# Kernel optimization log

Hardware: AMD Instinct MI355X
Metric: run time of the kernel (lower is better)

## Reference

```python
import jax, jax.numpy as jnp
import numpy as np

N = 50000
E = 800000
TEXT_VOCAB = 7000
ACTION_DIM = 64
MAX_POS = 5120
POS_DIM = 128   # edge encoder out_dim
NODE_DIM = 128  # text_out 64 + type_out 64
EDGE_DIM = 128
H1 = 256
OUT = 32
NEG_SLOPE = 0.2


def _pos_table():
    # sinusoidal table, [MAX_POS+1, POS_DIM]; even cols = cos, odd cols = sin
    positions = np.arange(0, MAX_POS + 1, dtype=np.float32)
    inv_freq = 1.0 / (10000.0 ** (np.arange(0.0, POS_DIM, 2.0, dtype=np.float32) / POS_DIM))
    si = np.outer(positions, inv_freq)
    tab = np.zeros((MAX_POS + 1, POS_DIM), dtype=np.float32)
    tab[:, 1::2] = np.sin(si)
    tab[:, 0::2] = np.cos(si)
    return jnp.asarray(tab)


def setup_inputs() -> dict:
    key = jax.random.key(0)
    ks = jax.random.split(key, 32)
    ri = jax.random.randint
    nrm = lambda k, s, scale=0.05: (jax.random.normal(k, s, dtype=jnp.float32) * scale)
    x = jnp.stack([ri(ks[0], (N,), 0, TEXT_VOCAB + 1, dtype=jnp.int32),
                   ri(ks[1], (N,), 0, 3, dtype=jnp.int32)], axis=-1)
    edge_index = ri(ks[2], (2, E), 0, N, dtype=jnp.int32)
    edge_attr = jnp.stack([ri(ks[3], (E,), 0, 3, dtype=jnp.int32),
                           ri(ks[4], (E,), 0, MAX_POS + 1, dtype=jnp.int32)], axis=-1)
    d = {
        "x": x, "edge_index": edge_index, "edge_attr": edge_attr,
        "text_emb": nrm(ks[5], (TEXT_VOCAB + 1, 64), 1.0),
        "type_emb": nrm(ks[6], (3, 64), 1.0),
        "flow_emb": nrm(ks[7], (3, EDGE_DIM), 1.0),
        "pos_table": _pos_table(),
        "pos_W": nrm(ks[8], (POS_DIM, POS_DIM)), "pos_b": nrm(ks[9], (POS_DIM,)),
        "c1_Wl": nrm(ks[10], (NODE_DIM, H1)), "c1_bl": nrm(ks[11], (H1,)),
        "c1_Wr": nrm(ks[12], (NODE_DIM, H1)), "c1_br": nrm(ks[13], (H1,)),
        "c1_We": nrm(ks[14], (EDGE_DIM, H1)), "c1_att": nrm(ks[15], (H1,)),
        "c1_bias": nrm(ks[16], (H1,)),
        "c2_Wl": nrm(ks[17], (H1, OUT)), "c2_bl": nrm(ks[18], (OUT,)),
        "c2_Wr": nrm(ks[19], (H1, OUT)), "c2_br": nrm(ks[20], (OUT,)),
        "c2_We": nrm(ks[21], (EDGE_DIM, OUT)), "c2_att": nrm(ks[22], (OUT,)),
        "c2_bias": nrm(ks[23], (OUT,)),
        "policy_W": nrm(ks[24], (OUT, ACTION_DIM), 0.2), "policy_b": nrm(ks[25], (ACTION_DIM,)),
    }
    return d


def gatv2(h, src, dst, ea, Wl, bl, Wr, br, We, att, bias, n):
    # PyG GATv2Conv, heads=1, add_self_loops=True, fill_value='mean'
    loop_attr = jnp.broadcast_to(ea.mean(0), (n, ea.shape[1]))
    s = jnp.concatenate([src, jnp.arange(n, dtype=src.dtype)])
    d = jnp.concatenate([dst, jnp.arange(n, dtype=dst.dtype)])
    ea_full = jnp.concatenate([ea, loop_attr], axis=0)
    xl = h @ Wl + bl  # messages (source side)
    xr = h @ Wr + br  # destination side
    m = xl[s] + xr[d] + ea_full @ We          # [E+n, F]
    e = jnp.where(m > 0, m, NEG_SLOPE * m) @ att  # per-edge logit [E+n]
    emax = jax.ops.segment_max(e, d, num_segments=n)
    a = jnp.exp(e - emax[d])
    denom = jax.ops.segment_sum(a, d, num_segments=n)
    alpha = a / denom[d]
    return jax.ops.segment_sum(alpha[:, None] * xl[s], d, num_segments=n) + bias


def reference(x, edge_index, edge_attr, text_emb, type_emb, flow_emb, pos_table,
              pos_W, pos_b,
              c1_Wl, c1_bl, c1_Wr, c1_br, c1_We, c1_att, c1_bias,
              c2_Wl, c2_bl, c2_Wr, c2_br, c2_We, c2_att, c2_bias,
              policy_W, policy_b):
    # NodeEncoder: concat of text and type embeddings -> [N, 128]
    h = jnp.concatenate([text_emb[x[:, 0]], type_emb[x[:, 1]]], axis=-1)
    # EdgeEncoder: flow embedding + linear(position sinusoid embedding)
    pos = edge_attr[:, 1]
    pos = jnp.where(pos > MAX_POS, pos, MAX_POS)  # faithful to original .where usage
    pos = jnp.clip(pos, 0, MAX_POS)
    ea = flow_emb[edge_attr[:, 0]] + (pos_table[pos] @ pos_W + pos_b)  # [E, 128]
    src, dst = edge_index[0], edge_index[1]
    h = gatv2(h, src, dst, ea, c1_Wl, c1_bl, c1_Wr, c1_br, c1_We, c1_att, c1_bias, h.shape[0])
    h = gatv2(h, src, dst, ea, c2_Wl, c2_bl, c2_Wr, c2_br, c2_We, c2_att, c2_bias, h.shape[0])
    g = h.mean(0)  # [32] graph readout
    logits = g @ policy_W + policy_b
    return jax.nn.softmax(logits, axis=-1)
```

## Files before the change

### kernel.cpp

```cpp
#include <hip/hip_runtime.h>

#define NEG_SLOPE 0.2f

typedef __attribute__((ext_vector_type(8))) short bf16x8;
typedef __attribute__((ext_vector_type(4))) float f32x4;

static __device__ __forceinline__ float lrelu(float m) {
    return fmaf(0.4f, fabsf(m), 0.6f * m);
}

static __device__ __forceinline__ float wsum64(float v) {
#pragma unroll
    for (int off = 32; off >= 1; off >>= 1) v += __shfl_xor(v, off, 64);
    return v;
}
static __device__ __forceinline__ float wsum32(float v) {
#pragma unroll
    for (int off = 16; off >= 1; off >>= 1) v += __shfl_xor(v, off, 64);
    return v;
}
static __device__ __forceinline__ float wmax64(float v) {
#pragma unroll
    for (int off = 32; off >= 1; off >>= 1) v = fmaxf(v, __shfl_xor(v, off, 64));
    return v;
}

static __device__ __forceinline__ unsigned short bf16r(float a) {
    unsigned int u = __float_as_uint(a);
    return (unsigned short)((u + 0x7FFFu + ((u >> 16) & 1u)) >> 16);
}
static __device__ __forceinline__ unsigned int bf16pack(float a, float b) {
    unsigned int ua = __float_as_uint(a);
    ua = (ua + 0x7FFFu + ((ua >> 16) & 1u)) >> 16;
    unsigned int ub = __float_as_uint(b);
    ub = (ub + 0x7FFFu + ((ub >> 16) & 1u)) & 0xFFFF0000u;
    return ua | ub;
}
static __device__ __forceinline__ float bfld(unsigned short s) {
    return __uint_as_float((unsigned int)s << 16);
}
static __device__ __forceinline__ float4 bf16x4_to_f4(uint2 u) {
    float4 v;
    v.x = __uint_as_float(u.x << 16);
    v.y = __uint_as_float(u.x & 0xFFFF0000u);
    v.z = __uint_as_float(u.y << 16);
    v.w = __uint_as_float(u.y & 0xFFFF0000u);
    return v;
}

static __device__ __forceinline__ float ldot4(const float4 xs, const float4 pre,
                                              const float4 av) {
    float q;
    q  = lrelu(xs.x + pre.x) * av.x;
    q += lrelu(xs.y + pre.y) * av.y;
    q += lrelu(xs.z + pre.z) * av.z;
    q += lrelu(xs.w + pre.w) * av.w;
    return q;
}

__global__ void k_zero_all(int* __restrict__ cntw, int n, int* __restrict__ cnt3,
                           int* __restrict__ gsum) {
    int i = blockIdx.x * blockDim.x + threadIdx.x;
    if (i < n) cntw[i] = 0;
    if (i < 4) cnt3[i] = 0;
    if (i < 32) gsum[i] = 0;
}

__global__ void k_edges(const int* __restrict__ ei, const int* __restrict__ ea,
                        int* __restrict__ cnt, int* __restrict__ cnt3, int E) {
    __shared__ int sh3[3];
    if (threadIdx.x < 3) sh3[threadIdx.x] = 0;
    __syncthreads();
    int e = blockIdx.x * blockDim.x + threadIdx.x;
    if (e < E) {
        atomicAdd(&cnt[ei[E + e]], 1);
        int f = ea[2 * e];
        f = f < 0 ? 0 : (f > 2 ? 2 : f);
        atomicAdd(&sh3[f], 1);
    }
    __syncthreads();
    if (threadIdx.x < 3) atomicAdd(&cnt3[threadIdx.x], sh3[threadIdx.x]);
}

__global__ void k_prep(const float* __restrict__ pos_table, const float* __restrict__ pos_W,
                       const float* __restrict__ pos_b, const float* __restrict__ flow_emb,
                       const float* __restrict__ We1, const float* __restrict__ We2,
                       const int* __restrict__ cnt3,
                       float* __restrict__ eaW1, float* __restrict__ loopW1,
                       float* __restrict__ eaW2, float* __restrict__ loopW2, int E) {
    __shared__ float posc[128];
    __shared__ float lv[128];
    int t = threadIdx.x;
    if (t < 128) {
        const float* row = pos_table + 5120 * 128;
        float a = pos_b[t];
        for (int k = 0; k < 128; ++k) a += row[k] * pos_W[k * 128 + t];
        posc[t] = a;
        float invE = 1.0f / (float)E;
        lv[t] = ((float)cnt3[0] * flow_emb[t] + (float)cnt3[1] * flow_emb[128 + t] +
                 (float)cnt3[2] * flow_emb[256 + t]) * invE + a;
    }
    __syncthreads();
    {
        int j = t;
        float a0 = 0.f, a1 = 0.f, a2 = 0.f, al = 0.f;
        for (int k = 0; k < 128; ++k) {
            float w = We1[k * 256 + j];
            float pc = posc[k];
            a0 += (flow_emb[k] + pc) * w;
            a1 += (flow_emb[128 + k] + pc) * w;
            a2 += (flow_emb[256 + k] + pc) * w;
            al += lv[k] * w;
        }
        eaW1[j] = a0; eaW1[256 + j] = a1; eaW1[512 + j] = a2; loopW1[j] = al;
    }
    if (t < 32) {
        int j = t;
        float a0 = 0.f, a1 = 0.f, a2 = 0.f, al = 0.f;
        for (int k = 0; k < 128; ++k) {
            float w = We2[k * 32 + j];
            float pc = posc[k];
            a0 += (flow_emb[k] + pc) * w;
            a1 += (flow_emb[128 + k] + pc) * w;
            a2 += (flow_emb[256 + k] + pc) * w;
            al += lv[k] * w;
        }
        eaW2[j] = a0; eaW2[32 + j] = a1; eaW2[64 + j] = a2; loopW2[j] = al;
    }
}

__global__ void k_prepW(const float* __restrict__ Wl1, const float* __restrict__ Wr1,
                        const float* __restrict__ Wl2, const float* __restrict__ Wr2,
                        unsigned short* __restrict__ Bt1, unsigned short* __restrict__ Bt2) {
    int i = blockIdx.x * blockDim.x + threadIdx.x;
    if (i < 512 * 128) {
        int nn = i >> 7, k = i & 127;
        float v = (nn < 256) ? Wl1[(size_t)k * 256 + nn] : Wr1[(size_t)k * 256 + nn - 256];
        Bt1[i] = bf16r(v);
    } else {
        int j = i - 512 * 128;
        if (j < 64 * 256) {
            int nn = j >> 8, k = j & 255;
            float v = (nn < 32) ? Wl2[(size_t)k * 32 + nn] : Wr2[(size_t)k * 32 + nn - 32];
            Bt2[j] = bf16r(v);
        }
    }
}

__global__ __launch_bounds__(256) void k_scan_block(const int* __restrict__ cnt,
                                                    int* __restrict__ rowptr,
                                                    int* __restrict__ bsum, int n) {
    __shared__ int sh[256];
    int b = blockIdx.x, t = threadIdx.x;
    int base = b * 1024 + t * 4;
    int v0 = base + 0 < n ? cnt[base + 0] : 0;
    int v1 = base + 1 < n ? cnt[base + 1] : 0;
    int v2 = base + 2 < n ? cnt[base + 2] : 0;
    int v3 = base + 3 < n ? cnt[base + 3] : 0;
    int tot = v0 + v1 + v2 + v3;
    sh[t] = tot;
    __syncthreads();
    for (int off = 1; off < 256; off <<= 1) {
        int x = (t >= off) ? sh[t - off] : 0;
        __syncthreads();
        sh[t] += x;
        __syncthreads();
    }
    int excl = (t > 0) ? sh[t - 1] : 0;
    if (base + 0 < n) rowptr[base + 0] = excl;
    if (base + 1 < n) rowptr[base + 1] = excl + v0;
    if (base + 2 < n) rowptr[base + 2] = excl + v0 + v1;
    if (base + 3 < n) rowptr[base + 3] = excl + v0 + v1 + v2;
    if (t == 255) bsum[b] = sh[255];
}

__global__ void k_scan_top(int* __restrict__ bsum, int* __restrict__ rowptr, int nb, int n) {
    if (threadIdx.x == 0 && blockIdx.x == 0) {
        int run = 0;
        for (int b = 0; b < nb; ++b) { int x = bsum[b]; bsum[b] = run; run += x; }
        rowptr[n] = run;
    }
}

__global__ void k_scan_add(int* __restrict__ rowptr, const int* __restrict__ bsum,
                           int* __restrict__ wptr, int n) {
    int i = blockIdx.x * blockDim.x + threadIdx.x;
    if (i < n) {
        int v = rowptr[i] + bsum[i >> 10];
        rowptr[i] = v;
        wptr[i] = v;
    }
}

__global__ void k_scatter(const int* __restrict__ ei, const int* __restrict__ ea,
                          int* __restrict__ wptr, int* __restrict__ packed, int E) {
    int e = blockIdx.x * blockDim.x + threadIdx.x;
    if (e >= E) return;
    int s = ei[e], d = ei[E + e];
    int f = ea[2 * e];
    f = f < 0 ? 0 : (f > 2 ? 2 : f);
    int p = atomicAdd(&wptr[d], 1);
    packed[p] = (s & 0xFFFF) | (f << 16);
}

__global__ __launch_bounds__(256) void k_gemm1(const int* __restrict__ x,
        const float* __restrict__ text_emb, const float* __restrict__ type_emb,
        const unsigned short* __restrict__ Bt,
        const float* __restrict__ bl, const float* __restrict__ br,
        unsigned short* __restrict__ xc, int n) {
    __shared__ unsigned short Ash[64][136];
    __shared__ unsigned short Bsh[128][136];
    int t = threadIdx.x;
    int node0 = blockIdx.x * 64;
    for (int i = t; i < 64 * 128; i += 256) {
        int r = i >> 7, cc = i & 127;
        int nd = node0 + r;
        float v = 0.f;
        if (nd < n)
            v = (cc < 64) ? text_emb[(size_t)x[nd * 2] * 64 + cc]
                          : type_emb[(size_t)x[nd * 2 + 1] * 64 + (cc - 64)];
        Ash[r][cc] = bf16r(v);
    }
    int wave = t >> 6, lane = t & 63;
    int m = lane & 15, q = lane >> 4;
    for (int nb = 0; nb < 4; ++nb) {
        __syncthreads();
        for (int i = t; i < 128 * 16; i += 256) {
            int r = i >> 4, cs = i & 15;
            uint4 v = ((const uint4*)(Bt + (size_t)(nb * 128 + r) * 128))[cs];
            *(uint4*)&Bsh[r][cs * 8] = v;
        }
        __syncthreads();
        f32x4 acc[8];
#pragma unroll
        for (int nt = 0; nt < 8; ++nt) acc[nt] = (f32x4){0.f, 0.f, 0.f, 0.f};
#pragma unroll
        for (int k = 0; k < 128; k += 32) {
            bf16x8 a = *(const bf16x8*)&Ash[wave * 16 + m][k + q * 8];
#pragma unroll
            for (int nt = 0; nt < 8; ++nt) {
                bf16x8 b = *(const bf16x8*)&Bsh[nt * 16 + m][k + q * 8];
                acc[nt] = __builtin_amdgcn_mfma_f32_16x16x32_bf16(a, b, acc[nt], 0, 0, 0);
            }
        }
#pragma unroll
        for (int r = 0; r < 4; ++r) {
            int node = node0 + wave * 16 + q * 4 + r;
            if (node < n) {
                unsigned short* rowp = xc + (size_t)node * 512 + nb * 128 + m;
#pragma unroll
                for (int nt = 0; nt < 8; ++nt) {
                    int ng = nb * 128 + nt * 16 + m;
                    float bv = (ng < 256) ? bl[ng] : br[ng - 256];
                    rowp[nt * 16] = bf16r(acc[nt][r] + bv);
                }
            }
        }
    }
}

__global__ __launch_bounds__(256) void k_gemm2(const unsigned short* __restrict__ h2b,
        const unsigned short* __restrict__ Bt,
        const float* __restrict__ bl, const float* __restrict__ br,
        unsigned short* __restrict__ xc, int n) {
    __shared__ unsigned short Ash[32][264];
    __shared__ unsigned short Bsh[64][264];
    int t = threadIdx.x;
    int node0 = blockIdx.x * 32;
    for (int i = t; i < 32 * 32; i += 256) {
        int r = i >> 5, cs = i & 31;
        int nd = node0 + r;
        uint4 v = make_uint4(0u, 0u, 0u, 0u);
        if (nd < n) v = ((const uint4*)(h2b + (size_t)nd * 256))[cs];
        *(uint4*)&Ash[r][cs * 8] = v;
    }
    for (int i = t; i < 64 * 32; i += 256) {
        int r = i >> 5, cs = i & 31;
        uint4 v = ((const uint4*)(Bt + (size_t)r * 256))[cs];
        *(uint4*)&Bsh[r][cs * 8] = v;
    }
    __syncthreads();
    int wave = t >> 6, lane = t & 63;
    int m = lane & 15, q = lane >> 4;
    int mrow = (wave >> 1) * 16;
    int nh   = (wave & 1) * 32;
    f32x4 acc[2];
    acc[0] = (f32x4){0.f, 0.f, 0.f, 0.f};
    acc[1] = (f32x4){0.f, 0.f, 0.f, 0.f};
#pragma unroll
    for (int k = 0; k < 256; k += 32) {
        bf16x8 a = *(const bf16x8*)&Ash[mrow + m][k + q * 8];
#pragma unroll
        for (int nt = 0; nt < 2; ++nt) {
            bf16x8 b = *(const bf16x8*)&Bsh[nh + nt * 16 + m][k + q * 8];
            acc[nt] = __builtin_amdgcn_mfma_f32_16x16x32_bf16(a, b, acc[nt], 0, 0, 0);
        }
    }
#pragma unroll
    for (int r = 0; r < 4; ++r) {
        int node = node0 + mrow + q * 4 + r;
        if (node < n) {
#pragma unroll
            for (int nt = 0; nt < 2; ++nt) {
                int ng = nh + nt * 16 + m;
                float bv = (ng < 32) ? bl[ng] : br[ng - 32];
                xc[(size_t)node * 64 + ng] = bf16r(acc[nt][r] + bv);
            }
        }
    }
}

__global__ __launch_bounds__(256) void k_gat256(const unsigned short* __restrict__ xc1,
        const int* __restrict__ rowptr, const int* __restrict__ packed,
        const float* __restrict__ eaW, const float* __restrict__ loopW,
        const float* __restrict__ att, const float* __restrict__ bias,
        unsigned short* __restrict__ h2b, int n) {
    int wid = (blockIdx.x * blockDim.x + threadIdx.x) >> 6;
    int lane = threadIdx.x & 63;
    if (wid >= n) return;
    int d = wid;
    int c = lane * 4;
    float4 xld = bf16x4_to_f4(((const uint2*)(xc1 + (size_t)d * 512))[lane]);
    float4 xrd = bf16x4_to_f4(((const uint2*)(xc1 + (size_t)d * 512 + 256))[lane]);
    float4 av  = *(const float4*)(att + c);
    float4 r0 = *(const float4*)(eaW + c);
    float4 r1 = *(const float4*)(eaW + 256 + c);
    float4 r2 = *(const float4*)(eaW + 512 + c);
    r0.x += xrd.x; r0.y += xrd.y; r0.z += xrd.z; r0.w += xrd.w;
    r1.x += xrd.x; r1.y += xrd.y; r1.z += xrd.z; r1.w += xrd.w;
    r2.x += xrd.x; r2.y += xrd.y; r2.z += xrd.z; r2.w += xrd.w;
    float4 lw = *(const float4*)(loopW + c);
    float4 sl; sl.x = xrd.x + lw.x; sl.y = xrd.y + lw.y;
    sl.z = xrd.z + lw.z; sl.w = xrd.w + lw.w;
    float q = wsum64(ldot4(xld, sl, av));
    float wself = __expf(q);
    float den = wself;
    float4 acc;
    acc.x = wself * xld.x; acc.y = wself * xld.y;
    acc.z = wself * xld.z; acc.w = wself * xld.w;

    int p0 = rowptr[d], p1 = rowptr[d + 1];
    int p = p0;
    for (; p + 4 <= p1; p += 4) {
        int pk0 = packed[p], pk1 = packed[p + 1];
        int pk2 = packed[p + 2], pk3 = packed[p + 3];
        uint2 u0 = ((const uint2*)(xc1 + (size_t)(pk0 & 0xFFFF) * 512))[lane];
        uint2 u1 = ((const uint2*)(xc1 + (size_t)(pk1 & 0xFFFF) * 512))[lane];
        uint2 u2 = ((const uint2*)(xc1 + (size_t)(pk2 & 0xFFFF) * 512))[lane];
        uint2 u3 = ((const uint2*)(xc1 + (size_t)(pk3 & 0xFFFF) * 512))[lane];
        float4 xs0 = bf16x4_to_f4(u0);
        float4 xs1 = bf16x4_to_f4(u1);
        float4 xs2 = bf16x4_to_f4(u2);
        float4 xs3 = bf16x4_to_f4(u3);
        int f0 = pk0 >> 16, f1 = pk1 >> 16, f2 = pk2 >> 16, f3 = pk3 >> 16;
        float4 pr0 = (f0 == 0) ? r0 : ((f0 == 1) ? r1 : r2);
        float4 pr1 = (f1 == 0) ? r0 : ((f1 == 1) ? r1 : r2);
        float4 pr2 = (f2 == 0) ? r0 : ((f2 == 1) ? r1 : r2);
        float4 pr3 = (f3 == 0) ? r0 : ((f3 == 1) ? r1 : r2);
        float q0 = ldot4(xs0, pr0, av);
        float q1 = ldot4(xs1, pr1, av);
        float q2 = ldot4(xs2, pr2, av);
        float q3 = ldot4(xs3, pr3, av);
#pragma unroll
        for (int off = 32; off >= 1; off >>= 1) {
            q0 += __shfl_xor(q0, off, 64);
            q1 += __shfl_xor(q1, off, 64);
            q2 += __shfl_xor(q2, off, 64);
            q3 += __shfl_xor(q3, off, 64);
        }
        float w0 = __expf(q0), w1 = __expf(q1);
        float w2 = __expf(q2), w3 = __expf(q3);
        den += (w0 + w1) + (w2 + w3);
        acc.x += w0 * xs0.x + w1 * xs1.x + w2 * xs2.x + w3 * xs3.x;
        acc.y += w0 * xs0.y + w1 * xs1.y + w2 * xs2.y + w3 * xs3.y;
        acc.z += w0 * xs0.z + w1 * xs1.z + w2 * xs2.z + w3 * xs3.z;
        acc.w += w0 * xs0.w + w1 * xs1.w + w2 * xs2.w + w3 * xs3.w;
    }
    for (; p < p1; ++p) {
        int pk = packed[p];
        float4 xs = bf16x4_to_f4(((const uint2*)(xc1 + (size_t)(pk & 0xFFFF) * 512))[lane]);
        int f = pk >> 16;
        float4 pr = (f == 0) ? r0 : ((f == 1) ? r1 : r2);
        float qq = wsum64(ldot4(xs, pr, av));
        float w = __expf(qq);
        den += w;
        acc.x += w * xs.x; acc.y += w * xs.y; acc.z += w * xs.z; acc.w += w * xs.w;
    }
    float inv = 1.f / den;
    float4 bv = *(const float4*)(bias + c);
    float4 o;
    o.x = acc.x * inv + bv.x; o.y = acc.y * inv + bv.y;
    o.z = acc.z * inv + bv.z; o.w = acc.w * inv + bv.w;
    ((uint2*)(h2b + (size_t)d * 256))[lane] =
        make_uint2(bf16pack(o.x, o.y), bf16pack(o.z, o.w));
}

__global__ __launch_bounds__(256) void k_gat32(const unsigned short* __restrict__ xc2,
        const int* __restrict__ rowptr, const int* __restrict__ packed,
        const float* __restrict__ eaW, const float* __restrict__ loopW,
        const float* __restrict__ att, const float* __restrict__ bias,
        float* __restrict__ out, int n) {
    int wid = (blockIdx.x * blockDim.x + threadIdx.x) >> 6;
    int lane = threadIdx.x & 63;
    if (wid >= n) return;
    int d = wid;
    int half = lane >> 5;
    int c = lane & 31;
    float xld = bfld(xc2[(size_t)d * 64 + c]);
    float xrd = bfld(xc2[(size_t)d * 64 + 32 + c]);
    float av = att[c];
    float r0 = eaW[c] + xrd, r1 = eaW[32 + c] + xrd, r2 = eaW[64 + c] + xrd;
    float den = 0.f, acc = 0.f;
    if (half == 0) {
        float lw = loopW[c];
        float q = wsum32(lrelu(xld + xrd + lw) * av);
        float wself = __expf(q);
        den = wself;
        acc = wself * xld;
    }
    int p0 = rowptr[d], p1 = rowptr[d + 1];
    int p = p0 + half;
    for (; p + 2 < p1; p += 4) {
        int pkA = packed[p], pkB = packed[p + 2];
        float xsA = bfld(xc2[(size_t)(pkA & 0xFFFF) * 64 + c]);
        float xsB = bfld(xc2[(size_t)(pkB & 0xFFFF) * 64 + c]);
        int fA = pkA >> 16, fB = pkB >> 16;
        float prA = (fA == 0) ? r0 : ((fA == 1) ? r1 : r2);
        float prB = (fB == 0) ? r0 : ((fB == 1) ? r1 : r2);
        float qA = lrelu(xsA + prA) * av;
        float qB = lrelu(xsB + prB) * av;
#pragma unroll
        for (int off = 16; off >= 1; off >>= 1) {
            qA += __shfl_xor(qA, off, 64);
            qB += __shfl_xor(qB, off, 64);
        }
        float wA = __expf(qA), wB = __expf(qB);
        den += wA + wB;
        acc += wA * xsA + wB * xsB;
    }
    for (; p < p1; p += 2) {
        int pk = packed[p];
        float xs = bfld(xc2[(size_t)(pk & 0xFFFF) * 64 + c]);
        int f = pk >> 16;
        float pr = (f == 0) ? r0 : ((f == 1) ? r1 : r2);
        float q = wsum32(lrelu(xs + pr) * av);
        float w = __expf(q);
        den += w;
        acc += w * xs;
    }
    den += __shfl_xor(den, 32, 64);
    acc += __shfl_xor(acc, 32, 64);
    if (lane < 32) out[(size_t)d * 32 + c] = acc / den + bias[c];
}

__global__ __launch_bounds__(256) void k_mean(const float* __restrict__ out2,
                                              float* __restrict__ gsum, int n) {
    __shared__ float sh[256];
    int t = threadIdx.x;
    int c = t & 31, g = t >> 5;
    float acc = 0.f;
    for (int nd = blockIdx.x * 8 + g; nd < n; nd += gridDim.x * 8)
        acc += out2[(size_t)nd * 32 + c];
    sh[t] = acc;
    __syncthreads();
    if (t < 32) {
        float s2 = 0.f;
#pragma unroll
        for (int gg = 0; gg < 8; ++gg) s2 += sh[gg * 32 + c];
        atomicAdd(&gsum[c], s2);
    }
}

__global__ void k_final(const float* __restrict__ gsum, const float* __restrict__ policy_W,
                        const float* __restrict__ policy_b, float* __restrict__ out, int n) {
    int t = threadIdx.x;
    float invN = 1.0f / (float)n;
    float acc = policy_b[t];
    for (int cc = 0; cc < 32; ++cc) acc += gsum[cc] * invN * policy_W[cc * 64 + t];
    float mx = wmax64(acc);
    float ex = __expf(acc - mx);
    float s = wsum64(ex);
    out[t] = ex / s;
}

extern "C" void kernel_launch(void* const* d_in, const int* in_sizes, int n_in,
                              void* d_out, int out_size, void* d_ws, size_t ws_size,
                              hipStream_t stream) {
    const int* x          = (const int*)d_in[0];
    const int* edge_index = (const int*)d_in[1];
    const int* edge_attr  = (const int*)d_in[2];
    const float* text_emb = (const float*)d_in[3];
    const float* type_emb = (const float*)d_in[4];
    const float* flow_emb = (const float*)d_in[5];
    const float* pos_table= (const float*)d_in[6];
    const float* pos_W    = (const float*)d_in[7];
    const float* pos_b    = (const float*)d_in[8];
    const float* c1_Wl    = (const float*)d_in[9];
    const float* c1_bl    = (const float*)d_in[10];
    const float* c1_Wr    = (const float*)d_in[11];
    const float* c1_br    = (const float*)d_in[12];
    const float* c1_We    = (const float*)d_in[13];
    const float* c1_att   = (const float*)d_in[14];
    const float* c1_bias  = (const float*)d_in[15];
    const float* c2_Wl    = (const float*)d_in[16];
    const float* c2_bl    = (const float*)d_in[17];
    const float* c2_Wr    = (const float*)d_in[18];
    const float* c2_br    = (const float*)d_in[19];
    const float* c2_We    = (const float*)d_in[20];
    const float* c2_att   = (const float*)d_in[21];
    const float* c2_bias  = (const float*)d_in[22];
    const float* policy_W = (const float*)d_in[23];
    const float* policy_b = (const float*)d_in[24];
    float* out = (float*)d_out;

    const int N = in_sizes[0] / 2;
    const int E = in_sizes[1] / 2;

    char* base = (char*)d_ws;
    size_t off = 0;
    auto alloc = [&](size_t bytes) -> void* {
        void* p = base + off;
        off = (off + bytes + 255) & ~(size_t)255;
        return p;
    };
    unsigned short* xc1  = (unsigned short*)alloc((size_t)N * 512 * 2);
    unsigned short* h2b  = (unsigned short*)alloc((size_t)N * 256 * 2);
    unsigned short* xc2  = (unsigned short*)alloc((size_t)N * 64 * 2);
    float*          out2 = (float*)alloc((size_t)N * 32 * 4);
    unsigned short* Bt1  = (unsigned short*)alloc((size_t)512 * 128 * 2);
    unsigned short* Bt2  = (unsigned short*)alloc((size_t)64 * 256 * 2);
    int*            cntw   = (int*)alloc((size_t)N * 4);
    int*            rowptr = (int*)alloc((size_t)(N + 1) * 4);
    int*            packed = (int*)alloc((size_t)E * 4);
    int*            bsum   = (int*)alloc(64 * 4);
    int*            cnt3   = (int*)alloc(4 * 4);
    float*          eaW1   = (float*)alloc(768 * 4);
    float*          loopW1 = (float*)alloc(256 * 4);
    float*          eaW2   = (float*)alloc(96 * 4);
    float*          loopW2 = (float*)alloc(32 * 4);
    float*          gsum   = (float*)alloc(32 * 4);

    k_zero_all<<<(N + 255) / 256, 256, 0, stream>>>(cntw, N, cnt3, (int*)gsum);

    k_edges<<<(E + 255) / 256, 256, 0, stream>>>(edge_index, edge_attr, cntw, cnt3, E);
    k_prep<<<1, 256, 0, stream>>>(pos_table, pos_W, pos_b, flow_emb, c1_We, c2_We,
                                  cnt3, eaW1, loopW1, eaW2, loopW2, E);
    k_prepW<<<(512 * 128 + 64 * 256 + 255) / 256, 256, 0, stream>>>(
        c1_Wl, c1_Wr, c2_Wl, c2_Wr, Bt1, Bt2);

    int nb = (N + 1023) / 1024;
    k_scan_block<<<nb, 256, 0, stream>>>(cntw, rowptr, bsum, N);
    k_scan_top<<<1, 64, 0, stream>>>(bsum, rowptr, nb, N);
    k_scan_add<<<(N + 255) / 256, 256, 0, stream>>>(rowptr, bsum, cntw, N);
    k_scatter<<<(E + 255) / 256, 256, 0, stream>>>(edge_index, edge_attr, cntw, packed, E);

    k_gemm1<<<(N + 63) / 64, 256, 0, stream>>>(x, text_emb, type_emb, Bt1,
                                               c1_bl, c1_br, xc1, N);
    k_gat256<<<(N + 3) / 4, 256, 0, stream>>>(xc1, rowptr, packed, eaW1, loopW1,
                                              c1_att, c1_bias, h2b, N);

    k_gemm2<<<(N + 31) / 32, 256, 0, stream>>>(h2b, Bt2, c2_bl, c2_br, xc2, N);
    k_gat32<<<(N + 3) / 4, 256, 0, stream>>>(xc2, rowptr, packed, eaW2, loopW2,
                                             c2_att, c2_bias, out2, N);

    k_mean<<<256, 256, 0, stream>>>(out2, gsum, N);
    k_final<<<1, 64, 0, stream>>>(gsum, policy_W, policy_b, out, N);
}
```

Before: 447.0 us.

## Bucket CSR by destination and flow type; restructure GAT edge loops

Builds the CSR keyed on (destination, flow type) so each GAT kernel walks three sub-ranges with a fixed edge-attribute term per range. This removes the per-edge flow select and packed-index decoding, so only the raw source index is stored. It also folds the leaky-ReLU constants into scaled attention vectors, and reorganises the 32-wide GAT to process four edges per wavefront with 16 lanes each. Weight prep is merged into one launch and zeroing becomes a single memset. The trade-off is a scan three times longer and extra loop overhead for short per-type segments.

```diff
diff --git a/kernel.cpp b/kernel.cpp
--- a/kernel.cpp
+++ b/kernel.cpp
@@ -5,18 +5,9 @@
 typedef __attribute__((ext_vector_type(8))) short bf16x8;
 typedef __attribute__((ext_vector_type(4))) float f32x4;
 
-static __device__ __forceinline__ float lrelu(float m) {
-    return fmaf(0.4f, fabsf(m), 0.6f * m);
-}
-
 static __device__ __forceinline__ float wsum64(float v) {
 #pragma unroll
     for (int off = 32; off >= 1; off >>= 1) v += __shfl_xor(v, off, 64);
-    return v;
-}
-static __device__ __forceinline__ float wsum32(float v) {
-#pragma unroll
-    for (int off = 16; off >= 1; off >>= 1) v += __shfl_xor(v, off, 64);
     return v;
 }
 static __device__ __forceinline__ float wmax64(float v) {
@@ -35,9 +26,6 @@
     unsigned int ub = __float_as_uint(b);
     ub = (ub + 0x7FFFu + ((ub >> 16) & 1u)) & 0xFFFF0000u;
     return ua | ub;
-}
-static __device__ __forceinline__ float bfld(unsigned short s) {
-    return __uint_as_float((unsigned int)s << 16);
 }
 static __device__ __forceinline__ float4 bf16x4_to_f4(uint2 u) {
     float4 v;
@@ -48,46 +36,60 @@
     return v;
 }
 
-static __device__ __forceinline__ float ldot4(const float4 xs, const float4 pre,
-                                              const float4 av) {
-    float q;
-    q  = lrelu(xs.x + pre.x) * av.x;
-    q += lrelu(xs.y + pre.y) * av.y;
-    q += lrelu(xs.z + pre.z) * av.z;
-    q += lrelu(xs.w + pre.w) * av.w;
+static __device__ __forceinline__ float sdot4(const float4 xs, const float4 pre,
+                                              const float4 av6, const float4 av4) {
+    float m0 = xs.x + pre.x, m1 = xs.y + pre.y;
+    float m2 = xs.z + pre.z, m3 = xs.w + pre.w;
+    float q = av6.x * m0 + av4.x * fabsf(m0);
+    q = fmaf(av6.y, m1, q); q = fmaf(av4.y, fabsf(m1), q);
+    q = fmaf(av6.z, m2, q); q = fmaf(av4.z, fabsf(m2), q);
+    q = fmaf(av6.w, m3, q); q = fmaf(av4.w, fabsf(m3), q);
     return q;
 }
 
-__global__ void k_zero_all(int* __restrict__ cntw, int n, int* __restrict__ cnt3,
-                           int* __restrict__ gsum) {
-    int i = blockIdx.x * blockDim.x + threadIdx.x;
-    if (i < n) cntw[i] = 0;
-    if (i < 4) cnt3[i] = 0;
-    if (i < 32) gsum[i] = 0;
-}
-
 __global__ void k_edges(const int* __restrict__ ei, const int* __restrict__ ea,
-                        int* __restrict__ cnt, int* __restrict__ cnt3, int E) {
+                        int* __restrict__ cntF, int* __restrict__ cnt3, int E) {
     __shared__ int sh3[3];
     if (threadIdx.x < 3) sh3[threadIdx.x] = 0;
     __syncthreads();
     int e = blockIdx.x * blockDim.x + threadIdx.x;
     if (e < E) {
-        atomicAdd(&cnt[ei[E + e]], 1);
+        int dd = ei[E + e];
         int f = ea[2 * e];
         f = f < 0 ? 0 : (f > 2 ? 2 : f);
+        atomicAdd(&cntF[dd * 3 + f], 1);
         atomicAdd(&sh3[f], 1);
     }
     __syncthreads();
     if (threadIdx.x < 3) atomicAdd(&cnt3[threadIdx.x], sh3[threadIdx.x]);
 }
 
-__global__ void k_prep(const float* __restrict__ pos_table, const float* __restrict__ pos_W,
-                       const float* __restrict__ pos_b, const float* __restrict__ flow_emb,
-                       const float* __restrict__ We1, const float* __restrict__ We2,
-                       const int* __restrict__ cnt3,
-                       float* __restrict__ eaW1, float* __restrict__ loopW1,
-                       float* __restrict__ eaW2, float* __restrict__ loopW2, int E) {
+__global__ void k_prep_all(const float* __restrict__ pos_table, const float* __restrict__ pos_W,
+                           const float* __restrict__ pos_b, const float* __restrict__ flow_emb,
+                           const float* __restrict__ We1, const float* __restrict__ We2,
+                           const int* __restrict__ cnt3,
+                           float* __restrict__ eaW1, float* __restrict__ loopW1,
+                           float* __restrict__ eaW2, float* __restrict__ loopW2,
+                           const float* __restrict__ Wl1, const float* __restrict__ Wr1,
+                           const float* __restrict__ Wl2, const float* __restrict__ Wr2,
+                           unsigned short* __restrict__ Bt1, unsigned short* __restrict__ Bt2,
+                           int E) {
+    if (blockIdx.x != 0) {
+        int i = (blockIdx.x - 1) * 256 + threadIdx.x;
+        if (i < 512 * 128) {
+            int nn = i >> 7, k = i & 127;
+            float v = (nn < 256) ? Wl1[(size_t)k * 256 + nn] : Wr1[(size_t)k * 256 + nn - 256];
+            Bt1[i] = bf16r(v);
+        } else {
+            int j = i - 512 * 128;
+            if (j < 64 * 256) {
+                int nn = j >> 8, k = j & 255;
+                float v = (nn < 32) ? Wl2[(size_t)k * 32 + nn] : Wr2[(size_t)k * 32 + nn - 32];
+                Bt2[j] = bf16r(v);
+            }
+        }
+        return;
+    }
     __shared__ float posc[128];
     __shared__ float lv[128];
     int t = threadIdx.x;
@@ -126,24 +128,6 @@
             al += lv[k] * w;
         }
         eaW2[j] = a0; eaW2[32 + j] = a1; eaW2[64 + j] = a2; loopW2[j] = al;
-    }
-}
-
-__global__ void k_prepW(const float* __restrict__ Wl1, const float* __restrict__ Wr1,
-                        const float* __restrict__ Wl2, const float* __restrict__ Wr2,
-                        unsigned short* __restrict__ Bt1, unsigned short* __restrict__ Bt2) {
-    int i = blockIdx.x * blockDim.x + threadIdx.x;
-    if (i < 512 * 128) {
-        int nn = i >> 7, k = i & 127;
-        float v = (nn < 256) ? Wl1[(size_t)k * 256 + nn] : Wr1[(size_t)k * 256 + nn - 256];
-        Bt1[i] = bf16r(v);
-    } else {
-        int j = i - 512 * 128;
-        if (j < 64 * 256) {
-            int nn = j >> 8, k = j & 255;
-            float v = (nn < 32) ? Wl2[(size_t)k * 32 + nn] : Wr2[(size_t)k * 32 + nn - 32];
-            Bt2[j] = bf16r(v);
-        }
     }
 }
 
@@ -196,11 +180,11 @@
                           int* __restrict__ wptr, int* __restrict__ packed, int E) {
     int e = blockIdx.x * blockDim.x + threadIdx.x;
     if (e >= E) return;
-    int s = ei[e], d = ei[E + e];
+    int s = ei[e], dd = ei[E + e];
     int f = ea[2 * e];
     f = f < 0 ? 0 : (f > 2 ? 2 : f);
-    int p = atomicAdd(&wptr[d], 1);
-    packed[p] = (s & 0xFFFF) | (f << 16);
+    int p = atomicAdd(&wptr[dd * 3 + f], 1);
+    packed[p] = s;
 }
 
 __global__ __launch_bounds__(256) void k_gemm1(const int* __restrict__ x,
@@ -311,7 +295,7 @@
 }
 
 __global__ __launch_bounds__(256) void k_gat256(const unsigned short* __restrict__ xc1,
-        const int* __restrict__ rowptr, const int* __restrict__ packed,
+        const int* __restrict__ rowptrF, const int* __restrict__ packed,
         const float* __restrict__ eaW, const float* __restrict__ loopW,
         const float* __restrict__ att, const float* __restrict__ bias,
         unsigned short* __restrict__ h2b, int n) {
@@ -322,135 +306,156 @@
     int c = lane * 4;
     float4 xld = bf16x4_to_f4(((const uint2*)(xc1 + (size_t)d * 512))[lane]);
     float4 xrd = bf16x4_to_f4(((const uint2*)(xc1 + (size_t)d * 512 + 256))[lane]);
-    float4 av  = *(const float4*)(att + c);
-    float4 r0 = *(const float4*)(eaW + c);
-    float4 r1 = *(const float4*)(eaW + 256 + c);
-    float4 r2 = *(const float4*)(eaW + 512 + c);
-    r0.x += xrd.x; r0.y += xrd.y; r0.z += xrd.z; r0.w += xrd.w;
-    r1.x += xrd.x; r1.y += xrd.y; r1.z += xrd.z; r1.w += xrd.w;
-    r2.x += xrd.x; r2.y += xrd.y; r2.z += xrd.z; r2.w += xrd.w;
-    float4 lw = *(const float4*)(loopW + c);
-    float4 sl; sl.x = xrd.x + lw.x; sl.y = xrd.y + lw.y;
-    sl.z = xrd.z + lw.z; sl.w = xrd.w + lw.w;
-    float q = wsum64(ldot4(xld, sl, av));
-    float wself = __expf(q);
-    float den = wself;
+    float4 av = *(const float4*)(att + c);
+    float4 av6, av4;
+    av6.x = 0.6f * av.x; av6.y = 0.6f * av.y; av6.z = 0.6f * av.z; av6.w = 0.6f * av.w;
+    av4.x = 0.4f * av.x; av4.y = 0.4f * av.y; av4.z = 0.4f * av.z; av4.w = 0.4f * av.w;
+    float den, wself;
     float4 acc;
-    acc.x = wself * xld.x; acc.y = wself * xld.y;
-    acc.z = wself * xld.z; acc.w = wself * xld.w;
-
-    int p0 = rowptr[d], p1 = rowptr[d + 1];
-    int p = p0;
-    for (; p + 4 <= p1; p += 4) {
-        int pk0 = packed[p], pk1 = packed[p + 1];
-        int pk2 = packed[p + 2], pk3 = packed[p + 3];
-        uint2 u0 = ((const uint2*)(xc1 + (size_t)(pk0 & 0xFFFF) * 512))[lane];
-        uint2 u1 = ((const uint2*)(xc1 + (size_t)(pk1 & 0xFFFF) * 512))[lane];
-        uint2 u2 = ((const uint2*)(xc1 + (size_t)(pk2 & 0xFFFF) * 512))[lane];
-        uint2 u3 = ((const uint2*)(xc1 + (size_t)(pk3 & 0xFFFF) * 512))[lane];
-        float4 xs0 = bf16x4_to_f4(u0);
-        float4 xs1 = bf16x4_to_f4(u1);
-        float4 xs2 = bf16x4_to_f4(u2);
-        float4 xs3 = bf16x4_to_f4(u3);
-        int f0 = pk0 >> 16, f1 = pk1 >> 16, f2 = pk2 >> 16, f3 = pk3 >> 16;
-        float4 pr0 = (f0 == 0) ? r0 : ((f0 == 1) ? r1 : r2);
-        float4 pr1 = (f1 == 0) ? r0 : ((f1 == 1) ? r1 : r2);
-        float4 pr2 = (f2 == 0) ? r0 : ((f2 == 1) ? r1 : r2);
-        float4 pr3 = (f3 == 0) ? r0 : ((f3 == 1) ? r1 : r2);
-        float q0 = ldot4(xs0, pr0, av);
-        float q1 = ldot4(xs1, pr1, av);
-        float q2 = ldot4(xs2, pr2, av);
-        float q3 = ldot4(xs3, pr3, av);
-#pragma unroll
-        for (int off = 32; off >= 1; off >>= 1) {
-            q0 += __shfl_xor(q0, off, 64);
-            q1 += __shfl_xor(q1, off, 64);
-            q2 += __shfl_xor(q2, off, 64);
-            q3 += __shfl_xor(q3, off, 64);
-        }
-        float w0 = __expf(q0), w1 = __expf(q1);
-        float w2 = __expf(q2), w3 = __expf(q3);
-        den += (w0 + w1) + (w2 + w3);
-        acc.x += w0 * xs0.x + w1 * xs1.x + w2 * xs2.x + w3 * xs3.x;
-        acc.y += w0 * xs0.y + w1 * xs1.y + w2 * xs2.y + w3 * xs3.y;
-        acc.z += w0 * xs0.z + w1 * xs1.z + w2 * xs2.z + w3 * xs3.z;
-        acc.w += w0 * xs0.w + w1 * xs1.w + w2 * xs2.w + w3 * xs3.w;
-    }
-    for (; p < p1; ++p) {
-        int pk = packed[p];
-        float4 xs = bf16x4_to_f4(((const uint2*)(xc1 + (size_t)(pk & 0xFFFF) * 512))[lane]);
-        int f = pk >> 16;
-        float4 pr = (f == 0) ? r0 : ((f == 1) ? r1 : r2);
-        float qq = wsum64(ldot4(xs, pr, av));
-        float w = __expf(qq);
-        den += w;
-        acc.x += w * xs.x; acc.y += w * xs.y; acc.z += w * xs.z; acc.w += w * xs.w;
+    {
+        float4 lw = *(const float4*)(loopW + c);
+        lw.x += xrd.x; lw.y += xrd.y; lw.z += xrd.z; lw.w += xrd.w;
+        float q = wsum64(sdot4(xld, lw, av6, av4));
+        wself = __expf(q);
+        den = wself;
+        acc.x = wself * xld.x; acc.y = wself * xld.y;
+        acc.z = wself * xld.z; acc.w = wself * xld.w;
+    }
+#pragma unroll 1
+    for (int f = 0; f < 3; ++f) {
+        float4 pre = *(const float4*)(eaW + f * 256 + c);
+        pre.x += xrd.x; pre.y += xrd.y; pre.z += xrd.z; pre.w += xrd.w;
+        int p = rowptrF[d * 3 + f], p1 = rowptrF[d * 3 + f + 1];
+        for (; p + 4 <= p1; p += 4) {
+            int s0 = packed[p],     s1 = packed[p + 1];
+            int s2 = packed[p + 2], s3 = packed[p + 3];
+            uint2 u0 = ((const uint2*)(xc1 + (size_t)s0 * 512))[lane];
+            uint2 u1 = ((const uint2*)(xc1 + (size_t)s1 * 512))[lane];
+            uint2 u2 = ((const uint2*)(xc1 + (size_t)s2 * 512))[lane];
+            uint2 u3 = ((const uint2*)(xc1 + (size_t)s3 * 512))[lane];
+            float4 xs0 = bf16x4_to_f4(u0);
+            float4 xs1 = bf16x4_to_f4(u1);
+            float4 xs2 = bf16x4_to_f4(u2);
+            float4 xs3 = bf16x4_to_f4(u3);
+            float q0 = sdot4(xs0, pre, av6, av4);
+            float q1 = sdot4(xs1, pre, av6, av4);
+            float q2 = sdot4(xs2, pre, av6, av4);
+            float q3 = sdot4(xs3, pre, av6, av4);
+#pragma unroll
+            for (int off = 32; off >= 1; off >>= 1) {
+                q0 += __shfl_xor(q0, off, 64);
+                q1 += __shfl_xor(q1, off, 64);
+                q2 += __shfl_xor(q2, off, 64);
+                q3 += __shfl_xor(q3, off, 64);
+            }
+            float w0 = __expf(q0), w1 = __expf(q1);
+            float w2 = __expf(q2), w3 = __expf(q3);
+            den += (w0 + w1) + (w2 + w3);
+            acc.x += w0 * xs0.x + w1 * xs1.x + w2 * xs2.x + w3 * xs3.x;
+            acc.y += w0 * xs0.y + w1 * xs1.y + w2 * xs2.y + w3 * xs3.y;
+            acc.z += w0 * xs0.z + w1 * xs1.z + w2 * xs2.z + w3 * xs3.z;
+            acc.w += w0 * xs0.w + w1 * xs1.w + w2 * xs2.w + w3 * xs3.w;
+        }
+        for (; p < p1; ++p) {
+            int s = packed[p];
+            float4 xs = bf16x4_to_f4(((const uint2*)(xc1 + (size_t)s * 512))[lane]);
+            float qq = wsum64(sdot4(xs, pre, av6, av4));
+            float w = __expf(qq);
+            den += w;
+            acc.x += w * xs.x; acc.y += w * xs.y; acc.z += w * xs.z; acc.w += w * xs.w;
+        }
     }
     float inv = 1.f / den;
     float4 bv = *(const float4*)(bias + c);
-    float4 o;
-    o.x = acc.x * inv + bv.x; o.y = acc.y * inv + bv.y;
-    o.z = acc.z * inv + bv.z; o.w = acc.w * inv + bv.w;
-    ((uint2*)(h2b + (size_t)d * 256))[lane] =
-        make_uint2(bf16pack(o.x, o.y), bf16pack(o.z, o.w));
+    float ox = fmaf(acc.x, inv, bv.x), oy = fmaf(acc.y, inv, bv.y);
+    float oz = fmaf(acc.z, inv, bv.z), ow = fmaf(acc.w, inv, bv.w);
+    ((uint2*)(h2b + (size_t)d * 256))[lane] = make_uint2(bf16pack(ox, oy), bf16pack(oz, ow));
 }
 
 __global__ __launch_bounds__(256) void k_gat32(const unsigned short* __restrict__ xc2,
-        const int* __restrict__ rowptr, const int* __restrict__ packed,
+        const int* __restrict__ rowptrF, const int* __restrict__ packed,
         const float* __restrict__ eaW, const float* __restrict__ loopW,
         const float* __restrict__ att, const float* __restrict__ bias,
         float* __restrict__ out, int n) {
     int wid = (blockIdx.x * blockDim.x + threadIdx.x) >> 6;
+    if (wid >= n) return;
     int lane = threadIdx.x & 63;
-    if (wid >= n) return;
+    int g = lane >> 4, li = lane & 15;
     int d = wid;
-    int half = lane >> 5;
-    int c = lane & 31;
-    float xld = bfld(xc2[(size_t)d * 64 + c]);
-    float xrd = bfld(xc2[(size_t)d * 64 + 32 + c]);
-    float av = att[c];
-    float r0 = eaW[c] + xrd, r1 = eaW[32 + c] + xrd, r2 = eaW[64 + c] + xrd;
-    float den = 0.f, acc = 0.f;
-    if (half == 0) {
-        float lw = loopW[c];
-        float q = wsum32(lrelu(xld + xrd + lw) * av);
+    unsigned int uxl = ((const unsigned int*)(xc2 + (size_t)d * 64))[li];
+    unsigned int uxr = ((const unsigned int*)(xc2 + (size_t)d * 64 + 32))[li];
+    float xl0 = __uint_as_float(uxl << 16), xl1 = __uint_as_float(uxl & 0xFFFF0000u);
+    float xr0 = __uint_as_float(uxr << 16), xr1 = __uint_as_float(uxr & 0xFFFF0000u);
+    float2 avv = ((const float2*)att)[li];
+    float a60 = 0.6f * avv.x, a61 = 0.6f * avv.y;
+    float a40 = 0.4f * avv.x, a41 = 0.4f * avv.y;
+    float den, acc0, acc1;
+    {
+        float2 lwv = ((const float2*)loopW)[li];
+        float m0 = xl0 + xr0 + lwv.x, m1 = xl1 + xr1 + lwv.y;
+        float q = a60 * m0 + a40 * fabsf(m0);
+        q = fmaf(a61, m1, q); q = fmaf(a41, fabsf(m1), q);
+        q += __shfl_xor(q, 1, 64); q += __shfl_xor(q, 2, 64);
+        q += __shfl_xor(q, 4, 64); q += __shfl_xor(q, 8, 64);
         float wself = __expf(q);
-        den = wself;
-        acc = wself * xld;
-    }
-    int p0 = rowptr[d], p1 = rowptr[d + 1];
-    int p = p0 + half;
-    for (; p + 2 < p1; p += 4) {
-        int pkA = packed[p], pkB = packed[p + 2];
-        float xsA = bfld(xc2[(size_t)(pkA & 0xFFFF) * 64 + c]);
-        float xsB = bfld(xc2[(size_t)(pkB & 0xFFFF) * 64 + c]);
-        int fA = pkA >> 16, fB = pkB >> 16;
-        float prA = (fA == 0) ? r0 : ((fA == 1) ? r1 : r2);
-        float prB = (fB == 0) ? r0 : ((fB == 1) ? r1 : r2);
-        float qA = lrelu(xsA + prA) * av;
-        float qB = lrelu(xsB + prB) * av;
-#pragma unroll
-        for (int off = 16; off >= 1; off >>= 1) {
-            qA += __shfl_xor(qA, off, 64);
-            qB += __shfl_xor(qB, off, 64);
-        }
-        float wA = __expf(qA), wB = __expf(qB);
-        den += wA + wB;
-        acc += wA * xsA + wB * xsB;
-    }
-    for (; p < p1; p += 2) {
-        int pk = packed[p];
-        float xs = bfld(xc2[(size_t)(pk & 0xFFFF) * 64 + c]);
-        int f = pk >> 16;
-        float pr = (f == 0) ? r0 : ((f == 1) ? r1 : r2);
-        float q = wsum32(lrelu(xs + pr) * av);
-        float w = __expf(q);
-        den += w;
-        acc += w * xs;
-    }
-    den += __shfl_xor(den, 32, 64);
-    acc += __shfl_xor(acc, 32, 64);
-    if (lane < 32) out[(size_t)d * 32 + c] = acc / den + bias[c];
+        den  = (g == 0) ? wself : 0.f;
+        acc0 = (g == 0) ? wself * xl0 : 0.f;
+        acc1 = (g == 0) ? wself * xl1 : 0.f;
+    }
+#pragma unroll 1
+    for (int f = 0; f < 3; ++f) {
+        float2 ev = ((const float2*)(eaW + f * 32))[li];
+        float pre0 = ev.x + xr0, pre1 = ev.y + xr1;
+        int pA = rowptrF[d * 3 + f], pB = rowptrF[d * 3 + f + 1];
+        int p = pA + g;
+        for (; p + 4 < pB; p += 8) {
+            int s0 = packed[p], s1 = packed[p + 4];
+            unsigned int ua = ((const unsigned int*)(xc2 + (size_t)s0 * 64))[li];
+            unsigned int ub = ((const unsigned int*)(xc2 + (size_t)s1 * 64))[li];
+            float xa0 = __uint_as_float(ua << 16), xa1 = __uint_as_float(ua & 0xFFFF0000u);
+            float xb0 = __uint_as_float(ub << 16), xb1 = __uint_as_float(ub & 0xFFFF0000u);
+            float ma0 = xa0 + pre0, ma1 = xa1 + pre1;
+            float mb0 = xb0 + pre0, mb1 = xb1 + pre1;
+            float qa = a60 * ma0 + a40 * fabsf(ma0);
+            qa = fmaf(a61, ma1, qa); qa = fmaf(a41, fabsf(ma1), qa);
+            float qb = a60 * mb0 + a40 * fabsf(mb0);
+            qb = fmaf(a61, mb1, qb); qb = fmaf(a41, fabsf(mb1), qb);
+#pragma unroll
+            for (int off = 1; off <= 8; off <<= 1) {
+                qa += __shfl_xor(qa, off, 64);
+                qb += __shfl_xor(qb, off, 64);
+            }
+            float wa = __expf(qa), wb = __expf(qb);
+            den += wa + wb;
+            acc0 = fmaf(wb, xb0, fmaf(wa, xa0, acc0));
+            acc1 = fmaf(wb, xb1, fmaf(wa, xa1, acc1));
+        }
+        for (; p < pB; p += 4) {
+            int s = packed[p];
+            unsigned int u = ((const unsigned int*)(xc2 + (size_t)s * 64))[li];
+            float x0 = __uint_as_float(u << 16), x1 = __uint_as_float(u & 0xFFFF0000u);
+            float m0 = x0 + pre0, m1 = x1 + pre1;
+            float q = a60 * m0 + a40 * fabsf(m0);
+            q = fmaf(a61, m1, q); q = fmaf(a41, fabsf(m1), q);
+            q += __shfl_xor(q, 1, 64); q += __shfl_xor(q, 2, 64);
+            q += __shfl_xor(q, 4, 64); q += __shfl_xor(q, 8, 64);
+            float w = __expf(q);
+            den += w;
+            acc0 = fmaf(w, x0, acc0);
+            acc1 = fmaf(w, x1, acc1);
+        }
+    }
+    acc0 += __shfl_xor(acc0, 16, 64); acc0 += __shfl_xor(acc0, 32, 64);
+    acc1 += __shfl_xor(acc1, 16, 64); acc1 += __shfl_xor(acc1, 32, 64);
+    den  += __shfl_xor(den, 16, 64);  den  += __shfl_xor(den, 32, 64);
+    if (g == 0) {
+        float2 bvv = ((const float2*)bias)[li];
+        float inv = 1.f / den;
+        float2 o;
+        o.x = fmaf(acc0, inv, bvv.x);
+        o.y = fmaf(acc1, inv, bvv.y);
+        ((float2*)(out + (size_t)d * 32))[li] = o;
+    }
 }
 
 __global__ __launch_bounds__(256) void k_mean(const float* __restrict__ out2,
@@ -515,6 +520,7 @@
 
     const int N = in_sizes[0] / 2;
     const int E = in_sizes[1] / 2;
+    const int n3 = 3 * N;
 
     char* base = (char*)d_ws;
     size_t off = 0;
@@ -529,38 +535,38 @@
     float*          out2 = (float*)alloc((size_t)N * 32 * 4);
     unsigned short* Bt1  = (unsigned short*)alloc((size_t)512 * 128 * 2);
     unsigned short* Bt2  = (unsigned short*)alloc((size_t)64 * 256 * 2);
-    int*            cntw   = (int*)alloc((size_t)N * 4);
-    int*            rowptr = (int*)alloc((size_t)(N + 1) * 4);
+    int*            zreg   = (int*)alloc((size_t)(n3 + 36) * 4);
+    int*            cntF   = zreg;
+    int*            cnt3   = zreg + n3;
+    float*          gsum   = (float*)(zreg + n3 + 4);
+    int*            rowptrF= (int*)alloc((size_t)(n3 + 1) * 4);
     int*            packed = (int*)alloc((size_t)E * 4);
-    int*            bsum   = (int*)alloc(64 * 4);
-    int*            cnt3   = (int*)alloc(4 * 4);
+    int*            bsum   = (int*)alloc(256 * 4);
     float*          eaW1   = (float*)alloc(768 * 4);
     float*          loopW1 = (float*)alloc(256 * 4);
     float*          eaW2   = (float*)alloc(96 * 4);
     float*          loopW2 = (float*)alloc(32 * 4);
-    float*          gsum   = (float*)alloc(32 * 4);
-
-    k_zero_all<<<(N + 255) / 256, 256, 0, stream>>>(cntw, N, cnt3, (int*)gsum);
-
-    k_edges<<<(E + 255) / 256, 256, 0, stream>>>(edge_index, edge_attr, cntw, cnt3, E);
-    k_prep<<<1, 256, 0, stream>>>(pos_table, pos_W, pos_b, flow_emb, c1_We, c2_We,
-                                  cnt3, eaW1, loopW1, eaW2, loopW2, E);
-    k_prepW<<<(512 * 128 + 64 * 256 + 255) / 256, 256, 0, stream>>>(
-        c1_Wl, c1_Wr, c2_Wl, c2_Wr, Bt1, Bt2);
-
-    int nb = (N + 1023) / 1024;
-    k_scan_block<<<nb, 256, 0, stream>>>(cntw, rowptr, bsum, N);
-    k_scan_top<<<1, 64, 0, stream>>>(bsum, rowptr, nb, N);
-    k_scan_add<<<(N + 255) / 256, 256, 0, stream>>>(rowptr, bsum, cntw, N);
-    k_scatter<<<(E + 255) / 256, 256, 0, stream>>>(edge_index, edge_attr, cntw, packed, E);
+
+    hipMemsetAsync(zreg, 0, (size_t)(n3 + 36) * 4, stream);
+
+    k_edges<<<(E + 255) / 256, 256, 0, stream>>>(edge_index, edge_attr, cntF, cnt3, E);
+    k_prep_all<<<1 + (512 * 128 + 64 * 256) / 256, 256, 0, stream>>>(
+        pos_table, pos_W, pos_b, flow_emb, c1_We, c2_We, cnt3,
+        eaW1, loopW1, eaW2, loopW2, c1_Wl, c1_Wr, c2_Wl, c2_Wr, Bt1, Bt2, E);
+
+    int nb = (n3 + 1023) / 1024;
+    k_scan_block<<<nb, 256, 0, stream>>>(cntF, rowptrF, bsum, n3);
+    k_scan_top<<<1, 64, 0, stream>>>(bsum, rowptrF, nb, n3);
+    k_scan_add<<<(n3 + 255) / 256, 256, 0, stream>>>(rowptrF, bsum, cntF, n3);
+    k_scatter<<<(E + 255) / 256, 256, 0, stream>>>(edge_index, edge_attr, cntF, packed, E);
 
     k_gemm1<<<(N + 63) / 64, 256, 0, stream>>>(x, text_emb, type_emb, Bt1,
                                                c1_bl, c1_br, xc1, N);
-    k_gat256<<<(N + 3) / 4, 256, 0, stream>>>(xc1, rowptr, packed, eaW1, loopW1,
+    k_gat256<<<(N + 3) / 4, 256, 0, stream>>>(xc1, rowptrF, packed, eaW1, loopW1,
                                               c1_att, c1_bias, h2b, N);
 
     k_gemm2<<<(N + 31) / 32, 256, 0, stream>>>(h2b, Bt2, c2_bl, c2_br, xc2, N);
-    k_gat32<<<(N + 3) / 4, 256, 0, stream>>>(xc2, rowptr, packed, eaW2, loopW2,
+    k_gat32<<<(N + 3) / 4, 256, 0, stream>>>(xc2, rowptrF, packed, eaW2, loopW2,
                                              c2_att, c2_bias, out2, N);
 
     k_mean<<<256, 256, 0, stream>>>(out2, gsum, N);
```

Result: slower. 470.2 us (+5.2%).
